# Kernel tuning notes

Hardware: AMD Instinct MI355X
Metric: run time of the kernel (lower is better)

The kernel has to match this reference:

```python
import jax, jax.numpy as jnp
import numpy as np

N_NODES = 100000
N_EDGES = 3200000
FEAT = 64  # pos(32) + vel(32)
OUT_DIM = 2


def setup_inputs() -> dict:
    key = jax.random.key(0)
    k1, k2, k3, k4, k5, k6, k7, k8 = jax.random.split(key, 8)
    pos = jax.random.normal(k1, (N_NODES, 32), dtype=jnp.float32)
    vel = jax.random.normal(k2, (N_NODES, 32), dtype=jnp.float32)
    edge_index = jax.random.randint(k3, (2, N_EDGES), 0, N_NODES, dtype=jnp.int64 if jax.config.jax_enable_x64 else jnp.int32)
    s = 1.0 / np.sqrt(FEAT)
    W_rel = jax.random.uniform(k4, (FEAT, FEAT), jnp.float32, -s, s)
    b_rel = jax.random.uniform(k5, (FEAT,), jnp.float32, -s, s)
    W_root = jax.random.uniform(k6, (FEAT, FEAT), jnp.float32, -s, s)
    W_pred = jax.random.uniform(k7, (FEAT, OUT_DIM), jnp.float32, -s, s)
    b_pred = jax.random.uniform(k8, (OUT_DIM,), jnp.float32, -s, s)
    return {"pos": pos, "vel": vel, "edge_index": edge_index,
            "W_rel": W_rel, "b_rel": b_rel, "W_root": W_root,
            "W_pred": W_pred, "b_pred": b_pred}


def reference(pos, vel, edge_index, W_rel, b_rel, W_root, W_pred, b_pred):
    # h = cat([pos, vel], -1)  -> [N, 64]
    h = jnp.concatenate([pos, vel], axis=-1)
    src, dst = edge_index[0], edge_index[1]
    # GraphConv (PyG, aggr='add'): out_i = lin_rel(sum_{j->i} h_j) + lin_root(h_i)
    msgs = h[src]  # [E, 64] irregular gather
    agg = jax.ops.segment_sum(msgs, dst, num_segments=N_NODES)  # [N, 64]
    conv_out = agg @ W_rel + b_rel + h @ W_root
    # lin_pred
    return conv_out @ W_pred + b_pred
```

## Files before the change

kernel.cpp:

```cpp
#include <hip/hip_runtime.h>

#define N_NODES 100000
#define N_EDGES 3200000
#define FEAT 64
#define OUT_DIM 2

#define SHIFT 8
#define S_NODES 256
#define K_BUCKETS 391
#define CAP 8704
#define NB 400
#define EPB (N_EDGES / NB)
#define BT 1024


__global__ __launch_bounds__(256) void node_kernel(const float* __restrict__ pos,
                                                   const float* __restrict__ vel,
                                                   const float* __restrict__ W_rel,
                                                   const float* __restrict__ b_rel,
                                                   const float* __restrict__ W_root,
                                                   const float* __restrict__ W_pred,
                                                   const float* __restrict__ b_pred,
                                                   float* __restrict__ y,
                                                   float* __restrict__ out,
                                                   int* __restrict__ gcount) {
    __shared__ float sM[258];
    int t = threadIdx.x;

    if (blockIdx.x == 0)
        for (int i = t; i < K_BUCKETS; i += 256) gcount[i] = 0;

    {
        const float* W = (t < 128) ? W_rel : W_root;
        int k = (t & 127) >> 1, o = t & 1;
        float acc = 0.f;
        #pragma unroll
        for (int f = 0; f < FEAT; ++f) acc += W[k * FEAT + f] * W_pred[f * OUT_DIM + o];
        sM[t] = acc;
        if (t < OUT_DIM) {
            float b = b_pred[t];
            #pragma unroll
            for (int f = 0; f < FEAT; ++f) b += b_rel[f] * W_pred[f * OUT_DIM + t];
            sM[256 + t] = b;
        }
    }
    __syncthreads();

    int n = blockIdx.x * 256 + t;
    if (n >= N_NODES) return;

    const float4* p4 = (const float4*)(pos + (size_t)n * 32);
    const float4* v4 = (const float4*)(vel + (size_t)n * 32);
    float h[FEAT];
    #pragma unroll
    for (int i = 0; i < 8; ++i) {
        float4 a = p4[i];
        h[i * 4 + 0] = a.x; h[i * 4 + 1] = a.y; h[i * 4 + 2] = a.z; h[i * 4 + 3] = a.w;
    }
    #pragma unroll
    for (int i = 0; i < 8; ++i) {
        float4 a = v4[i];
        h[32 + i * 4 + 0] = a.x; h[32 + i * 4 + 1] = a.y; h[32 + i * 4 + 2] = a.z; h[32 + i * 4 + 3] = a.w;
    }

    float rel0 = 0.f, rel1 = 0.f, ro0 = 0.f, ro1 = 0.f;
    #pragma unroll
    for (int k = 0; k < FEAT; ++k) {
        float hk = h[k];
        rel0 += hk * sM[2 * k + 0];
        rel1 += hk * sM[2 * k + 1];
        ro0  += hk * sM[128 + 2 * k + 0];
        ro1  += hk * sM[128 + 2 * k + 1];
    }
    ((float2*)y)[n]   = make_float2(rel0, rel1);
    ((float2*)out)[n] = make_float2(ro0 + sM[256], ro1 + sM[257]);
}

__global__ __launch_bounds__(BT) void binscatter_kernel(const int* __restrict__ edges,
                                                        int* __restrict__ gcount,
                                                        unsigned* __restrict__ scat) {
    __shared__ int hist[K_BUCKETS];
    __shared__ int cum[K_BUCKETS + 1];
    __shared__ int base[K_BUCKETS];
    __shared__ int pos[K_BUCKETS];
    __shared__ unsigned sortbuf[EPB];

    int t = threadIdx.x;
    for (int i = t; i < K_BUCKETS; i += BT) hist[i] = 0;
    __syncthreads();

    const int4* s4 = (const int4*)(edges) + blockIdx.x * (EPB / 4);
    const int4* d4 = (const int4*)(edges + N_EDGES) + blockIdx.x * (EPB / 4);
    int4 sreg[2], dreg[2];
    bool valid[2];
    #pragma unroll
    for (int r = 0; r < 2; ++r) {
        int i = t + r * BT;
        valid[r] = (i < EPB / 4);
        if (valid[r]) { sreg[r] = s4[i]; dreg[r] = d4[i]; }
    }

    #pragma unroll
    for (int r = 0; r < 2; ++r) {
        if (!valid[r]) continue;
        int4 d = dreg[r];
        atomicAdd(&hist[d.x >> SHIFT], 1);
        atomicAdd(&hist[d.y >> SHIFT], 1);
        atomicAdd(&hist[d.z >> SHIFT], 1);
        atomicAdd(&hist[d.w >> SHIFT], 1);
    }
    __syncthreads();

    for (int i = t; i < K_BUCKETS; i += BT) base[i] = atomicAdd(&gcount[i], hist[i]);
    if (t < 64) {
        int lo = t * 7;
        int vals[7];
        int lsum = 0;
        #pragma unroll
        for (int j = 0; j < 7; ++j) {
            int idx = lo + j;
            int v = (idx < K_BUCKETS) ? hist[idx] : 0;
            vals[j] = lsum;
            lsum += v;
        }
        int x = lsum;
        #pragma unroll
        for (int d = 1; d < 64; d <<= 1) {
            int up = __shfl_up(x, d);
            if (t >= d) x += up;
        }
        int excl = x - lsum;
        #pragma unroll
        for (int j = 0; j < 7; ++j) {
            int idx = lo + j;
            if (idx < K_BUCKETS) { cum[idx] = excl + vals[j]; pos[idx] = excl + vals[j]; }
        }
        if (t == 63) cum[K_BUCKETS] = excl + lsum;
    }
    __syncthreads();

    #pragma unroll
    for (int r = 0; r < 2; ++r) {
        if (!valid[r]) continue;
        int4 s = sreg[r];
        int4 d = dreg[r];
        int k, p;
        k = d.x >> SHIFT; p = atomicAdd(&pos[k], 1);
        sortbuf[p] = (unsigned)s.x | ((unsigned)(d.x & (S_NODES - 1)) << 17);
        k = d.y >> SHIFT; p = atomicAdd(&pos[k], 1);
        sortbuf[p] = (unsigned)s.y | ((unsigned)(d.y & (S_NODES - 1)) << 17);
        k = d.z >> SHIFT; p = atomicAdd(&pos[k], 1);
        sortbuf[p] = (unsigned)s.z | ((unsigned)(d.z & (S_NODES - 1)) << 17);
        k = d.w >> SHIFT; p = atomicAdd(&pos[k], 1);
        sortbuf[p] = (unsigned)s.w | ((unsigned)(d.w & (S_NODES - 1)) << 17);
    }
    __syncthreads();

    int wid = t >> 6, lane = t & 63;
    for (int k = wid; k < K_BUCKETS; k += BT / 64) {
        int s0 = cum[k], s1 = cum[k + 1], b = base[k];
        for (int j = s0 + lane; j < s1; j += 64) {
            int p = b + (j - s0);
            if (p < CAP) scat[(size_t)k * CAP + p] = sortbuf[j];
        }
    }
}

__global__ __launch_bounds__(BT) void accum_kernel(const unsigned* __restrict__ scat,
                                                   const int* __restrict__ gcount,
                                                   const float* __restrict__ y,
                                                   float* __restrict__ out) {
    __shared__ float acc[S_NODES * 2];
    int t = threadIdx.x;
    if (t < S_NODES * 2) acc[t] = 0.f;
    __syncthreads();

    int k = blockIdx.x;
    int c = gcount[k];
    if (c > CAP) c = CAP;
    const unsigned* sl = scat + (size_t)k * CAP;
    const float2* y2 = (const float2*)y;
    for (int i = t; i < c; i += BT) {
        unsigned p = sl[i];
        int src = p & 0x1FFFF;
        int dl = p >> 17;
        float2 v = y2[src];
        atomicAdd(&acc[dl], v.x);
        atomicAdd(&acc[S_NODES + dl], v.y);
    }
    __syncthreads();

    if (t < S_NODES) {
        int node = k * S_NODES + t;
        if (node < N_NODES) {
            float2* o2 = (float2*)out;
            float2 cv = o2[node];
            cv.x += acc[t];
            cv.y += acc[S_NODES + t];
            o2[node] = cv;
        }
    }
}

extern "C" void kernel_launch(void* const* d_in, const int* in_sizes, int n_in,
                              void* d_out, int out_size, void* d_ws, size_t ws_size,
                              hipStream_t stream) {
    const float* pos    = (const float*)d_in[0];
    const float* vel    = (const float*)d_in[1];
    const int*   edges  = (const int*)d_in[2];
    const float* W_rel  = (const float*)d_in[3];
    const float* b_rel  = (const float*)d_in[4];
    const float* W_root = (const float*)d_in[5];
    const float* W_pred = (const float*)d_in[6];
    const float* b_pred = (const float*)d_in[7];
    float* out = (float*)d_out;

    char* ws = (char*)d_ws;
    float*    y      = (float*)(ws + 2048);
    int*      gcount = (int*)(ws + 802048);
    unsigned* scat   = (unsigned*)(ws + 803712);

    int node_blocks = (N_NODES + 255) / 256;
    node_kernel<<<node_blocks, 256, 0, stream>>>(pos, vel, W_rel, b_rel, W_root,
                                                 W_pred, b_pred, y, out, gcount);

    binscatter_kernel<<<NB, BT, 0, stream>>>(edges, gcount, scat);

    accum_kernel<<<K_BUCKETS, BT, 0, stream>>>(scat, gcount, y, out);
}
```

Baseline: 165.5 us.

## Fuse node projection and edge binning into one launch; batch accum gathers

Merges the node projection kernel and the edge bucket-scatter kernel into a single launch. The first 98 blocks do the node work, the rest bin the edges, and shared memory is unioned between the two roles. Zeroing gcount moves to a memset. The accumulation kernel now loads packed edges as uint4 and issues all y gathers before the shared-memory atomics, which raises memory-level parallelism. The risks are an added memset launch, 1024-thread node blocks with fewer blocks in flight, and a fixed unroll of three uint4 loads per thread that relies on CAP fitting in 3*1024*4 entries.

```diff
diff --git a/kernel.cpp b/kernel.cpp
--- a/kernel.cpp
+++ b/kernel.cpp
@@ -12,85 +12,86 @@
 #define NB 400
 #define EPB (N_EDGES / NB)
 #define BT 1024
-
-
-__global__ __launch_bounds__(256) void node_kernel(const float* __restrict__ pos,
+#define NODE_BLOCKS 98
+
+
+__global__ __launch_bounds__(BT) void fused_kernel(const float* __restrict__ pos,
                                                    const float* __restrict__ vel,
                                                    const float* __restrict__ W_rel,
                                                    const float* __restrict__ b_rel,
                                                    const float* __restrict__ W_root,
                                                    const float* __restrict__ W_pred,
                                                    const float* __restrict__ b_pred,
+                                                   const int* __restrict__ edges,
+                                                   int* __restrict__ gcount,
+                                                   unsigned* __restrict__ scat,
                                                    float* __restrict__ y,
-                                                   float* __restrict__ out,
-                                                   int* __restrict__ gcount) {
-    __shared__ float sM[258];
+                                                   float* __restrict__ out) {
+    __shared__ union {
+        float sM[258];
+        struct {
+            int hist[K_BUCKETS];
+            int cum[K_BUCKETS + 1];
+            int base[K_BUCKETS];
+            int rpos[K_BUCKETS];
+            unsigned sortbuf[EPB];
+        } b;
+    } sm;
+
     int t = threadIdx.x;
 
-    if (blockIdx.x == 0)
-        for (int i = t; i < K_BUCKETS; i += 256) gcount[i] = 0;
-
-    {
-        const float* W = (t < 128) ? W_rel : W_root;
-        int k = (t & 127) >> 1, o = t & 1;
-        float acc = 0.f;
-        #pragma unroll
-        for (int f = 0; f < FEAT; ++f) acc += W[k * FEAT + f] * W_pred[f * OUT_DIM + o];
-        sM[t] = acc;
-        if (t < OUT_DIM) {
-            float b = b_pred[t];
+    if (blockIdx.x < NODE_BLOCKS) {
+        if (t < 256) {
+            const float* W = (t < 128) ? W_rel : W_root;
+            int k = (t & 127) >> 1, o = t & 1;
+            float acc = 0.f;
             #pragma unroll
-            for (int f = 0; f < FEAT; ++f) b += b_rel[f] * W_pred[f * OUT_DIM + t];
-            sM[256 + t] = b;
-        }
-    }
-    __syncthreads();
-
-    int n = blockIdx.x * 256 + t;
-    if (n >= N_NODES) return;
-
-    const float4* p4 = (const float4*)(pos + (size_t)n * 32);
-    const float4* v4 = (const float4*)(vel + (size_t)n * 32);
-    float h[FEAT];
-    #pragma unroll
-    for (int i = 0; i < 8; ++i) {
-        float4 a = p4[i];
-        h[i * 4 + 0] = a.x; h[i * 4 + 1] = a.y; h[i * 4 + 2] = a.z; h[i * 4 + 3] = a.w;
-    }
-    #pragma unroll
-    for (int i = 0; i < 8; ++i) {
-        float4 a = v4[i];
-        h[32 + i * 4 + 0] = a.x; h[32 + i * 4 + 1] = a.y; h[32 + i * 4 + 2] = a.z; h[32 + i * 4 + 3] = a.w;
-    }
-
-    float rel0 = 0.f, rel1 = 0.f, ro0 = 0.f, ro1 = 0.f;
-    #pragma unroll
-    for (int k = 0; k < FEAT; ++k) {
-        float hk = h[k];
-        rel0 += hk * sM[2 * k + 0];
-        rel1 += hk * sM[2 * k + 1];
-        ro0  += hk * sM[128 + 2 * k + 0];
-        ro1  += hk * sM[128 + 2 * k + 1];
-    }
-    ((float2*)y)[n]   = make_float2(rel0, rel1);
-    ((float2*)out)[n] = make_float2(ro0 + sM[256], ro1 + sM[257]);
-}
-
-__global__ __launch_bounds__(BT) void binscatter_kernel(const int* __restrict__ edges,
-                                                        int* __restrict__ gcount,
-                                                        unsigned* __restrict__ scat) {
-    __shared__ int hist[K_BUCKETS];
-    __shared__ int cum[K_BUCKETS + 1];
-    __shared__ int base[K_BUCKETS];
-    __shared__ int pos[K_BUCKETS];
-    __shared__ unsigned sortbuf[EPB];
-
-    int t = threadIdx.x;
-    for (int i = t; i < K_BUCKETS; i += BT) hist[i] = 0;
-    __syncthreads();
-
-    const int4* s4 = (const int4*)(edges) + blockIdx.x * (EPB / 4);
-    const int4* d4 = (const int4*)(edges + N_EDGES) + blockIdx.x * (EPB / 4);
+            for (int f = 0; f < FEAT; ++f) acc += W[k * FEAT + f] * W_pred[f * OUT_DIM + o];
+            sm.sM[t] = acc;
+            if (t < OUT_DIM) {
+                float b = b_pred[t];
+                #pragma unroll
+                for (int f = 0; f < FEAT; ++f) b += b_rel[f] * W_pred[f * OUT_DIM + t];
+                sm.sM[256 + t] = b;
+            }
+        }
+        __syncthreads();
+
+        int n = blockIdx.x * BT + t;
+        if (n >= N_NODES) return;
+
+        const float4* p4 = (const float4*)(pos + (size_t)n * 32);
+        const float4* v4 = (const float4*)(vel + (size_t)n * 32);
+        float rel0 = 0.f, rel1 = 0.f, ro0 = 0.f, ro1 = 0.f;
+        #pragma unroll
+        for (int i = 0; i < 8; ++i) {
+            float4 a = p4[i];
+            int k0 = i * 4;
+            rel0 += a.x * sm.sM[2*(k0+0)] + a.y * sm.sM[2*(k0+1)] + a.z * sm.sM[2*(k0+2)] + a.w * sm.sM[2*(k0+3)];
+            rel1 += a.x * sm.sM[2*(k0+0)+1] + a.y * sm.sM[2*(k0+1)+1] + a.z * sm.sM[2*(k0+2)+1] + a.w * sm.sM[2*(k0+3)+1];
+            ro0  += a.x * sm.sM[128+2*(k0+0)] + a.y * sm.sM[128+2*(k0+1)] + a.z * sm.sM[128+2*(k0+2)] + a.w * sm.sM[128+2*(k0+3)];
+            ro1  += a.x * sm.sM[128+2*(k0+0)+1] + a.y * sm.sM[128+2*(k0+1)+1] + a.z * sm.sM[128+2*(k0+2)+1] + a.w * sm.sM[128+2*(k0+3)+1];
+        }
+        #pragma unroll
+        for (int i = 0; i < 8; ++i) {
+            float4 a = v4[i];
+            int k0 = 32 + i * 4;
+            rel0 += a.x * sm.sM[2*(k0+0)] + a.y * sm.sM[2*(k0+1)] + a.z * sm.sM[2*(k0+2)] + a.w * sm.sM[2*(k0+3)];
+            rel1 += a.x * sm.sM[2*(k0+0)+1] + a.y * sm.sM[2*(k0+1)+1] + a.z * sm.sM[2*(k0+2)+1] + a.w * sm.sM[2*(k0+3)+1];
+            ro0  += a.x * sm.sM[128+2*(k0+0)] + a.y * sm.sM[128+2*(k0+1)] + a.z * sm.sM[128+2*(k0+2)] + a.w * sm.sM[128+2*(k0+3)];
+            ro1  += a.x * sm.sM[128+2*(k0+0)+1] + a.y * sm.sM[128+2*(k0+1)+1] + a.z * sm.sM[128+2*(k0+2)+1] + a.w * sm.sM[128+2*(k0+3)+1];
+        }
+        ((float2*)y)[n]   = make_float2(rel0, rel1);
+        ((float2*)out)[n] = make_float2(ro0 + sm.sM[256], ro1 + sm.sM[257]);
+        return;
+    }
+
+    int bb = blockIdx.x - NODE_BLOCKS;
+    for (int i = t; i < K_BUCKETS; i += BT) sm.b.hist[i] = 0;
+    __syncthreads();
+
+    const int4* s4 = (const int4*)(edges) + bb * (EPB / 4);
+    const int4* d4 = (const int4*)(edges + N_EDGES) + bb * (EPB / 4);
     int4 sreg[2], dreg[2];
     bool valid[2];
     #pragma unroll
@@ -104,14 +105,14 @@
     for (int r = 0; r < 2; ++r) {
         if (!valid[r]) continue;
         int4 d = dreg[r];
-        atomicAdd(&hist[d.x >> SHIFT], 1);
-        atomicAdd(&hist[d.y >> SHIFT], 1);
-        atomicAdd(&hist[d.z >> SHIFT], 1);
-        atomicAdd(&hist[d.w >> SHIFT], 1);
-    }
-    __syncthreads();
-
-    for (int i = t; i < K_BUCKETS; i += BT) base[i] = atomicAdd(&gcount[i], hist[i]);
+        atomicAdd(&sm.b.hist[d.x >> SHIFT], 1);
+        atomicAdd(&sm.b.hist[d.y >> SHIFT], 1);
+        atomicAdd(&sm.b.hist[d.z >> SHIFT], 1);
+        atomicAdd(&sm.b.hist[d.w >> SHIFT], 1);
+    }
+    __syncthreads();
+
+    for (int i = t; i < K_BUCKETS; i += BT) sm.b.base[i] = atomicAdd(&gcount[i], sm.b.hist[i]);
     if (t < 64) {
         int lo = t * 7;
         int vals[7];
@@ -119,7 +120,7 @@
         #pragma unroll
         for (int j = 0; j < 7; ++j) {
             int idx = lo + j;
-            int v = (idx < K_BUCKETS) ? hist[idx] : 0;
+            int v = (idx < K_BUCKETS) ? sm.b.hist[idx] : 0;
             vals[j] = lsum;
             lsum += v;
         }
@@ -133,9 +134,9 @@
         #pragma unroll
         for (int j = 0; j < 7; ++j) {
             int idx = lo + j;
-            if (idx < K_BUCKETS) { cum[idx] = excl + vals[j]; pos[idx] = excl + vals[j]; }
-        }
-        if (t == 63) cum[K_BUCKETS] = excl + lsum;
+            if (idx < K_BUCKETS) { sm.b.cum[idx] = excl + vals[j]; sm.b.rpos[idx] = excl + vals[j]; }
+        }
+        if (t == 63) sm.b.cum[K_BUCKETS] = excl + lsum;
     }
     __syncthreads();
 
@@ -145,23 +146,23 @@
         int4 s = sreg[r];
         int4 d = dreg[r];
         int k, p;
-        k = d.x >> SHIFT; p = atomicAdd(&pos[k], 1);
-        sortbuf[p] = (unsigned)s.x | ((unsigned)(d.x & (S_NODES - 1)) << 17);
-        k = d.y >> SHIFT; p = atomicAdd(&pos[k], 1);
-        sortbuf[p] = (unsigned)s.y | ((unsigned)(d.y & (S_NODES - 1)) << 17);
-        k = d.z >> SHIFT; p = atomicAdd(&pos[k], 1);
-        sortbuf[p] = (unsigned)s.z | ((unsigned)(d.z & (S_NODES - 1)) << 17);
-        k = d.w >> SHIFT; p = atomicAdd(&pos[k], 1);
-        sortbuf[p] = (unsigned)s.w | ((unsigned)(d.w & (S_NODES - 1)) << 17);
+        k = d.x >> SHIFT; p = atomicAdd(&sm.b.rpos[k], 1);
+        sm.b.sortbuf[p] = (unsigned)s.x | ((unsigned)(d.x & (S_NODES - 1)) << 17);
+        k = d.y >> SHIFT; p = atomicAdd(&sm.b.rpos[k], 1);
+        sm.b.sortbuf[p] = (unsigned)s.y | ((unsigned)(d.y & (S_NODES - 1)) << 17);
+        k = d.z >> SHIFT; p = atomicAdd(&sm.b.rpos[k], 1);
+        sm.b.sortbuf[p] = (unsigned)s.z | ((unsigned)(d.z & (S_NODES - 1)) << 17);
+        k = d.w >> SHIFT; p = atomicAdd(&sm.b.rpos[k], 1);
+        sm.b.sortbuf[p] = (unsigned)s.w | ((unsigned)(d.w & (S_NODES - 1)) << 17);
     }
     __syncthreads();
 
     int wid = t >> 6, lane = t & 63;
     for (int k = wid; k < K_BUCKETS; k += BT / 64) {
-        int s0 = cum[k], s1 = cum[k + 1], b = base[k];
+        int s0 = sm.b.cum[k], s1 = sm.b.cum[k + 1], b = sm.b.base[k];
         for (int j = s0 + lane; j < s1; j += 64) {
             int p = b + (j - s0);
-            if (p < CAP) scat[(size_t)k * CAP + p] = sortbuf[j];
+            if (p < CAP) scat[(size_t)k * CAP + p] = sm.b.sortbuf[j];
         }
     }
 }
@@ -170,23 +171,50 @@
                                                    const int* __restrict__ gcount,
                                                    const float* __restrict__ y,
                                                    float* __restrict__ out) {
-    __shared__ float acc[S_NODES * 2];
+    __shared__ float accx[S_NODES], accy[S_NODES];
     int t = threadIdx.x;
-    if (t < S_NODES * 2) acc[t] = 0.f;
+    if (t < S_NODES) { accx[t] = 0.f; accy[t] = 0.f; }
     __syncthreads();
 
     int k = blockIdx.x;
     int c = gcount[k];
     if (c > CAP) c = CAP;
-    const unsigned* sl = scat + (size_t)k * CAP;
+    const uint4* sl4 = (const uint4*)(scat + (size_t)k * CAP);
+    int nq = (c + 3) >> 2;
+
+    uint4 q0, q1, q2;
+    int i0 = t, i1 = t + BT, i2 = t + 2 * BT;
+    bool g0 = i0 < nq, g1 = i1 < nq, g2 = i2 < nq;
+    if (g0) q0 = sl4[i0];
+    if (g1) q1 = sl4[i1];
+    if (g2) q2 = sl4[i2];
+
     const float2* y2 = (const float2*)y;
-    for (int i = t; i < c; i += BT) {
-        unsigned p = sl[i];
-        int src = p & 0x1FFFF;
-        int dl = p >> 17;
-        float2 v = y2[src];
-        atomicAdd(&acc[dl], v.x);
-        atomicAdd(&acc[S_NODES + dl], v.y);
+    float2 v00, v01, v02, v03, v10, v11, v12, v13, v20, v21, v22, v23;
+    if (g0) { v00 = y2[q0.x & 0x1FFFF]; v01 = y2[q0.y & 0x1FFFF]; v02 = y2[q0.z & 0x1FFFF]; v03 = y2[q0.w & 0x1FFFF]; }
+    if (g1) { v10 = y2[q1.x & 0x1FFFF]; v11 = y2[q1.y & 0x1FFFF]; v12 = y2[q1.z & 0x1FFFF]; v13 = y2[q1.w & 0x1FFFF]; }
+    if (g2) { v20 = y2[q2.x & 0x1FFFF]; v21 = y2[q2.y & 0x1FFFF]; v22 = y2[q2.z & 0x1FFFF]; v23 = y2[q2.w & 0x1FFFF]; }
+
+    if (g0) {
+        int b = i0 << 2;
+        if (b + 0 < c) { atomicAdd(&accx[q0.x >> 17], v00.x); atomicAdd(&accy[q0.x >> 17], v00.y); }
+        if (b + 1 < c) { atomicAdd(&accx[q0.y >> 17], v01.x); atomicAdd(&accy[q0.y >> 17], v01.y); }
+        if (b + 2 < c) { atomicAdd(&accx[q0.z >> 17], v02.x); atomicAdd(&accy[q0.z >> 17], v02.y); }
+        if (b + 3 < c) { atomicAdd(&accx[q0.w >> 17], v03.x); atomicAdd(&accy[q0.w >> 17], v03.y); }
+    }
+    if (g1) {
+        int b = i1 << 2;
+        if (b + 0 < c) { atomicAdd(&accx[q1.x >> 17], v10.x); atomicAdd(&accy[q1.x >> 17], v10.y); }
+        if (b + 1 < c) { atomicAdd(&accx[q1.y >> 17], v11.x); atomicAdd(&accy[q1.y >> 17], v11.y); }
+        if (b + 2 < c) { atomicAdd(&accx[q1.z >> 17], v12.x); atomicAdd(&accy[q1.z >> 17], v12.y); }
+        if (b + 3 < c) { atomicAdd(&accx[q1.w >> 17], v13.x); atomicAdd(&accy[q1.w >> 17], v13.y); }
+    }
+    if (g2) {
+        int b = i2 << 2;
+        if (b + 0 < c) { atomicAdd(&accx[q2.x >> 17], v20.x); atomicAdd(&accy[q2.x >> 17], v20.y); }
+        if (b + 1 < c) { atomicAdd(&accx[q2.y >> 17], v21.x); atomicAdd(&accy[q2.y >> 17], v21.y); }
+        if (b + 2 < c) { atomicAdd(&accx[q2.z >> 17], v22.x); atomicAdd(&accy[q2.z >> 17], v22.y); }
+        if (b + 3 < c) { atomicAdd(&accx[q2.w >> 17], v23.x); atomicAdd(&accy[q2.w >> 17], v23.y); }
     }
     __syncthreads();
 
@@ -195,8 +223,8 @@
         if (node < N_NODES) {
             float2* o2 = (float2*)out;
             float2 cv = o2[node];
-            cv.x += acc[t];
-            cv.y += acc[S_NODES + t];
+            cv.x += accx[t];
+            cv.y += accy[t];
             o2[node] = cv;
         }
     }
@@ -220,11 +248,11 @@
     int*      gcount = (int*)(ws + 802048);
     unsigned* scat   = (unsigned*)(ws + 803712);
 
-    int node_blocks = (N_NODES + 255) / 256;
-    node_kernel<<<node_blocks, 256, 0, stream>>>(pos, vel, W_rel, b_rel, W_root,
-                                                 W_pred, b_pred, y, out, gcount);
-
-    binscatter_kernel<<<NB, BT, 0, stream>>>(edges, gcount, scat);
+    hipMemsetAsync(gcount, 0, K_BUCKETS * sizeof(int), stream);
+
+    fused_kernel<<<NODE_BLOCKS + NB, BT, 0, stream>>>(pos, vel, W_rel, b_rel, W_root,
+                                                      W_pred, b_pred, edges, gcount,
+                                                      scat, y, out);
 
     accum_kernel<<<K_BUCKETS, BT, 0, stream>>>(scat, gcount, y, out);
 }
```

Measured after the change: 168.1 us. No clear change (+1.6%).

## Fuse node, bin-scatter and accumulate stages into one cooperative kernel

Applied to the files above, without the earlier changes.

Merges the three launches into a single cooperative kernel of 256 blocks that separates the histogram, scatter and accumulate phases with grid-wide syncs. The bucketing changes to 256 buckets of 391 nodes each, so each block owns one bucket, keeps its root projection in registers, and writes the output once instead of doing a read-modify-write. The accumulate phase reads the scatter list with vectorized uint4 loads. It removes launch gaps and one pass over the output, but adds two grid barriers and a large shared-memory footprint per block, and keeps the three-kernel path as a fallback if the cooperative launch fails.

```diff
diff --git a/kernel.cpp b/kernel.cpp
--- a/kernel.cpp
+++ b/kernel.cpp
@@ -1,192 +1,362 @@
 #include <hip/hip_runtime.h>
+#include <hip/hip_cooperative_groups.h>
+
+namespace cg = cooperative_groups;
 
 #define N_NODES 100000
 #define N_EDGES 3200000
 #define FEAT 64
 #define OUT_DIM 2
 
-#define SHIFT 8
-#define S_NODES 256
-#define K_BUCKETS 391
-#define CAP 8704
-#define NB 400
-#define EPB (N_EDGES / NB)
+#define S_NODES 391
+#define K_BUCKETS 256
+#define CAP 13072
+#define GRID 256
 #define BT 1024
-
-
-__global__ __launch_bounds__(256) void node_kernel(const float* __restrict__ pos,
-                                                   const float* __restrict__ vel,
-                                                   const float* __restrict__ W_rel,
-                                                   const float* __restrict__ b_rel,
-                                                   const float* __restrict__ W_root,
-                                                   const float* __restrict__ W_pred,
-                                                   const float* __restrict__ b_pred,
-                                                   float* __restrict__ y,
-                                                   float* __restrict__ out,
-                                                   int* __restrict__ gcount) {
-    __shared__ float sM[258];
-    int t = threadIdx.x;
-
-    if (blockIdx.x == 0)
-        for (int i = t; i < K_BUCKETS; i += 256) gcount[i] = 0;
-
-    {
+#define EPB 12500
+#define NQ 3125
+#define V3LIM 53
+#define FB_NODE_BLOCKS 98
+
+
+__device__ __forceinline__ unsigned pack_edge(int s, int d) {
+    unsigned k = (unsigned)d / S_NODES;
+    unsigned dl = (unsigned)d - k * S_NODES;
+    return (unsigned)s | (dl << 17);
+}
+
+__device__ __forceinline__ void fold_weights(int t,
+        const float* __restrict__ W_rel, const float* __restrict__ b_rel,
+        const float* __restrict__ W_root, const float* __restrict__ W_pred,
+        const float* __restrict__ b_pred, float* sMl) {
+    if (t < 256) {
         const float* W = (t < 128) ? W_rel : W_root;
         int k = (t & 127) >> 1, o = t & 1;
         float acc = 0.f;
         #pragma unroll
         for (int f = 0; f < FEAT; ++f) acc += W[k * FEAT + f] * W_pred[f * OUT_DIM + o];
-        sM[t] = acc;
+        sMl[t] = acc;
         if (t < OUT_DIM) {
-            float b = b_pred[t];
+            float bb = b_pred[t];
             #pragma unroll
-            for (int f = 0; f < FEAT; ++f) b += b_rel[f] * W_pred[f * OUT_DIM + t];
-            sM[256 + t] = b;
-        }
-    }
-    __syncthreads();
-
-    int n = blockIdx.x * 256 + t;
-    if (n >= N_NODES) return;
-
+            for (int f = 0; f < FEAT; ++f) bb += b_rel[f] * W_pred[f * OUT_DIM + t];
+            sMl[256 + t] = bb;
+        }
+    }
+}
+
+__device__ __forceinline__ void node_dot(int n, const float* sMl,
+        const float* __restrict__ pos, const float* __restrict__ vel,
+        float* __restrict__ y, float* rx, float* ry) {
     const float4* p4 = (const float4*)(pos + (size_t)n * 32);
     const float4* v4 = (const float4*)(vel + (size_t)n * 32);
-    float h[FEAT];
+    float rel0 = 0.f, rel1 = 0.f, ro0 = 0.f, ro1 = 0.f;
     #pragma unroll
     for (int i = 0; i < 8; ++i) {
         float4 a = p4[i];
-        h[i * 4 + 0] = a.x; h[i * 4 + 1] = a.y; h[i * 4 + 2] = a.z; h[i * 4 + 3] = a.w;
+        int k0 = i * 4;
+        rel0 += a.x*sMl[2*k0]       + a.y*sMl[2*k0+2]     + a.z*sMl[2*k0+4]     + a.w*sMl[2*k0+6];
+        rel1 += a.x*sMl[2*k0+1]     + a.y*sMl[2*k0+3]     + a.z*sMl[2*k0+5]     + a.w*sMl[2*k0+7];
+        ro0  += a.x*sMl[128+2*k0]   + a.y*sMl[128+2*k0+2] + a.z*sMl[128+2*k0+4] + a.w*sMl[128+2*k0+6];
+        ro1  += a.x*sMl[128+2*k0+1] + a.y*sMl[128+2*k0+3] + a.z*sMl[128+2*k0+5] + a.w*sMl[128+2*k0+7];
     }
     #pragma unroll
     for (int i = 0; i < 8; ++i) {
         float4 a = v4[i];
-        h[32 + i * 4 + 0] = a.x; h[32 + i * 4 + 1] = a.y; h[32 + i * 4 + 2] = a.z; h[32 + i * 4 + 3] = a.w;
-    }
-
-    float rel0 = 0.f, rel1 = 0.f, ro0 = 0.f, ro1 = 0.f;
-    #pragma unroll
-    for (int k = 0; k < FEAT; ++k) {
-        float hk = h[k];
-        rel0 += hk * sM[2 * k + 0];
-        rel1 += hk * sM[2 * k + 1];
-        ro0  += hk * sM[128 + 2 * k + 0];
-        ro1  += hk * sM[128 + 2 * k + 1];
-    }
-    ((float2*)y)[n]   = make_float2(rel0, rel1);
-    ((float2*)out)[n] = make_float2(ro0 + sM[256], ro1 + sM[257]);
-}
-
-__global__ __launch_bounds__(BT) void binscatter_kernel(const int* __restrict__ edges,
-                                                        int* __restrict__ gcount,
-                                                        unsigned* __restrict__ scat) {
+        int k0 = 32 + i * 4;
+        rel0 += a.x*sMl[2*k0]       + a.y*sMl[2*k0+2]     + a.z*sMl[2*k0+4]     + a.w*sMl[2*k0+6];
+        rel1 += a.x*sMl[2*k0+1]     + a.y*sMl[2*k0+3]     + a.z*sMl[2*k0+5]     + a.w*sMl[2*k0+7];
+        ro0  += a.x*sMl[128+2*k0]   + a.y*sMl[128+2*k0+2] + a.z*sMl[128+2*k0+4] + a.w*sMl[128+2*k0+6];
+        ro1  += a.x*sMl[128+2*k0+1] + a.y*sMl[128+2*k0+3] + a.z*sMl[128+2*k0+5] + a.w*sMl[128+2*k0+7];
+    }
+    ((float2*)y)[n] = make_float2(rel0, rel1);
+    *rx = ro0 + sMl[256];
+    *ry = ro1 + sMl[257];
+}
+
+__global__ __launch_bounds__(BT, 4) void mega_kernel(
+        const float* __restrict__ pos, const float* __restrict__ vel,
+        const float* __restrict__ W_rel, const float* __restrict__ b_rel,
+        const float* __restrict__ W_root, const float* __restrict__ W_pred,
+        const float* __restrict__ b_pred, const int* __restrict__ edges,
+        int* __restrict__ gcount, unsigned* __restrict__ scat,
+        float* __restrict__ y, float* __restrict__ out) {
+    __shared__ float sMl[258];
     __shared__ int hist[K_BUCKETS];
     __shared__ int cum[K_BUCKETS + 1];
     __shared__ int base[K_BUCKETS];
-    __shared__ int pos[K_BUCKETS];
+    __shared__ int rpos[K_BUCKETS];
     __shared__ unsigned sortbuf[EPB];
-
-    int t = threadIdx.x;
+    __shared__ float accx[S_NODES], accy[S_NODES];
+
+    cg::grid_group grid = cg::this_grid();
+    const int t = threadIdx.x;
+    const int b = blockIdx.x;
+
     for (int i = t; i < K_BUCKETS; i += BT) hist[i] = 0;
-    __syncthreads();
-
-    const int4* s4 = (const int4*)(edges) + blockIdx.x * (EPB / 4);
-    const int4* d4 = (const int4*)(edges + N_EDGES) + blockIdx.x * (EPB / 4);
-    int4 sreg[2], dreg[2];
-    bool valid[2];
-    #pragma unroll
-    for (int r = 0; r < 2; ++r) {
-        int i = t + r * BT;
-        valid[r] = (i < EPB / 4);
-        if (valid[r]) { sreg[r] = s4[i]; dreg[r] = d4[i]; }
-    }
-
-    #pragma unroll
-    for (int r = 0; r < 2; ++r) {
-        if (!valid[r]) continue;
-        int4 d = dreg[r];
-        atomicAdd(&hist[d.x >> SHIFT], 1);
-        atomicAdd(&hist[d.y >> SHIFT], 1);
-        atomicAdd(&hist[d.z >> SHIFT], 1);
-        atomicAdd(&hist[d.w >> SHIFT], 1);
-    }
-    __syncthreads();
-
+
+    const int4* d4 = (const int4*)(edges + N_EDGES) + b * NQ;
+    int4 dreg0 = d4[t], dreg1 = d4[t + BT], dreg2 = d4[t + 2 * BT];
+    const bool v3 = t < V3LIM;
+    int4 dreg3;
+    if (v3) dreg3 = d4[t + 3 * BT];
+
+    if (b == 0)
+        for (int i = t; i < K_BUCKETS; i += BT) gcount[i] = 0;
+    __syncthreads();
+
+    atomicAdd(&hist[(unsigned)dreg0.x / S_NODES], 1);
+    atomicAdd(&hist[(unsigned)dreg0.y / S_NODES], 1);
+    atomicAdd(&hist[(unsigned)dreg0.z / S_NODES], 1);
+    atomicAdd(&hist[(unsigned)dreg0.w / S_NODES], 1);
+    atomicAdd(&hist[(unsigned)dreg1.x / S_NODES], 1);
+    atomicAdd(&hist[(unsigned)dreg1.y / S_NODES], 1);
+    atomicAdd(&hist[(unsigned)dreg1.z / S_NODES], 1);
+    atomicAdd(&hist[(unsigned)dreg1.w / S_NODES], 1);
+    atomicAdd(&hist[(unsigned)dreg2.x / S_NODES], 1);
+    atomicAdd(&hist[(unsigned)dreg2.y / S_NODES], 1);
+    atomicAdd(&hist[(unsigned)dreg2.z / S_NODES], 1);
+    atomicAdd(&hist[(unsigned)dreg2.w / S_NODES], 1);
+    if (v3) {
+        atomicAdd(&hist[(unsigned)dreg3.x / S_NODES], 1);
+        atomicAdd(&hist[(unsigned)dreg3.y / S_NODES], 1);
+        atomicAdd(&hist[(unsigned)dreg3.z / S_NODES], 1);
+        atomicAdd(&hist[(unsigned)dreg3.w / S_NODES], 1);
+    }
+
+    __threadfence();
+    grid.sync();
+    __threadfence();
+
+    fold_weights(t, W_rel, b_rel, W_root, W_pred, b_pred, sMl);
     for (int i = t; i < K_BUCKETS; i += BT) base[i] = atomicAdd(&gcount[i], hist[i]);
     if (t < 64) {
-        int lo = t * 7;
-        int vals[7];
-        int lsum = 0;
-        #pragma unroll
-        for (int j = 0; j < 7; ++j) {
-            int idx = lo + j;
-            int v = (idx < K_BUCKETS) ? hist[idx] : 0;
-            vals[j] = lsum;
-            lsum += v;
-        }
+        int lo = t * 4;
+        int vals[4]; int lsum = 0;
+        #pragma unroll
+        for (int j = 0; j < 4; ++j) { int v = hist[lo + j]; vals[j] = lsum; lsum += v; }
         int x = lsum;
         #pragma unroll
-        for (int d = 1; d < 64; d <<= 1) {
-            int up = __shfl_up(x, d);
-            if (t >= d) x += up;
-        }
+        for (int dd = 1; dd < 64; dd <<= 1) { int up = __shfl_up(x, dd); if (t >= dd) x += up; }
         int excl = x - lsum;
         #pragma unroll
-        for (int j = 0; j < 7; ++j) {
-            int idx = lo + j;
-            if (idx < K_BUCKETS) { cum[idx] = excl + vals[j]; pos[idx] = excl + vals[j]; }
-        }
+        for (int j = 0; j < 4; ++j) { cum[lo + j] = excl + vals[j]; rpos[lo + j] = excl + vals[j]; }
         if (t == 63) cum[K_BUCKETS] = excl + lsum;
     }
     __syncthreads();
 
+    float rootx = 0.f, rooty = 0.f;
+    const int n = b * S_NODES + t;
+    if (t < S_NODES && n < N_NODES)
+        node_dot(n, sMl, pos, vel, y, &rootx, &rooty);
+
+    const int4* s4 = (const int4*)(edges) + b * NQ;
+    int4 sreg0 = s4[t], sreg1 = s4[t + BT], sreg2 = s4[t + 2 * BT];
+    int4 sreg3;
+    if (v3) sreg3 = s4[t + 3 * BT];
+    {
+        int k, p;
+        k = (unsigned)dreg0.x / S_NODES; p = atomicAdd(&rpos[k], 1); sortbuf[p] = pack_edge(sreg0.x, dreg0.x);
+        k = (unsigned)dreg0.y / S_NODES; p = atomicAdd(&rpos[k], 1); sortbuf[p] = pack_edge(sreg0.y, dreg0.y);
+        k = (unsigned)dreg0.z / S_NODES; p = atomicAdd(&rpos[k], 1); sortbuf[p] = pack_edge(sreg0.z, dreg0.z);
+        k = (unsigned)dreg0.w / S_NODES; p = atomicAdd(&rpos[k], 1); sortbuf[p] = pack_edge(sreg0.w, dreg0.w);
+        k = (unsigned)dreg1.x / S_NODES; p = atomicAdd(&rpos[k], 1); sortbuf[p] = pack_edge(sreg1.x, dreg1.x);
+        k = (unsigned)dreg1.y / S_NODES; p = atomicAdd(&rpos[k], 1); sortbuf[p] = pack_edge(sreg1.y, dreg1.y);
+        k = (unsigned)dreg1.z / S_NODES; p = atomicAdd(&rpos[k], 1); sortbuf[p] = pack_edge(sreg1.z, dreg1.z);
+        k = (unsigned)dreg1.w / S_NODES; p = atomicAdd(&rpos[k], 1); sortbuf[p] = pack_edge(sreg1.w, dreg1.w);
+        k = (unsigned)dreg2.x / S_NODES; p = atomicAdd(&rpos[k], 1); sortbuf[p] = pack_edge(sreg2.x, dreg2.x);
+        k = (unsigned)dreg2.y / S_NODES; p = atomicAdd(&rpos[k], 1); sortbuf[p] = pack_edge(sreg2.y, dreg2.y);
+        k = (unsigned)dreg2.z / S_NODES; p = atomicAdd(&rpos[k], 1); sortbuf[p] = pack_edge(sreg2.z, dreg2.z);
+        k = (unsigned)dreg2.w / S_NODES; p = atomicAdd(&rpos[k], 1); sortbuf[p] = pack_edge(sreg2.w, dreg2.w);
+        if (v3) {
+            k = (unsigned)dreg3.x / S_NODES; p = atomicAdd(&rpos[k], 1); sortbuf[p] = pack_edge(sreg3.x, dreg3.x);
+            k = (unsigned)dreg3.y / S_NODES; p = atomicAdd(&rpos[k], 1); sortbuf[p] = pack_edge(sreg3.y, dreg3.y);
+            k = (unsigned)dreg3.z / S_NODES; p = atomicAdd(&rpos[k], 1); sortbuf[p] = pack_edge(sreg3.z, dreg3.z);
+            k = (unsigned)dreg3.w / S_NODES; p = atomicAdd(&rpos[k], 1); sortbuf[p] = pack_edge(sreg3.w, dreg3.w);
+        }
+    }
+    __syncthreads();
+
+    {
+        int wid = t >> 6, lane = t & 63;
+        for (int k = wid; k < K_BUCKETS; k += BT / 64) {
+            int s0 = cum[k], s1 = cum[k + 1], gb = base[k];
+            for (int j = s0 + lane; j < s1; j += 64) {
+                int p = gb + (j - s0);
+                if (p < CAP) scat[(size_t)k * CAP + p] = sortbuf[j];
+            }
+        }
+    }
+
+    __threadfence();
+    grid.sync();
+    __threadfence();
+
+    if (t < S_NODES) { accx[t] = 0.f; accy[t] = 0.f; }
+    __syncthreads();
+
+    int c = gcount[b];
+    if (c > CAP) c = CAP;
+    const int nq = (c + 3) >> 2;
+    const uint4* sl4 = (const uint4*)(scat + (size_t)b * CAP);
+    const float2* y2 = (const float2*)y;
     #pragma unroll
-    for (int r = 0; r < 2; ++r) {
-        if (!valid[r]) continue;
-        int4 s = sreg[r];
-        int4 d = dreg[r];
-        int k, p;
-        k = d.x >> SHIFT; p = atomicAdd(&pos[k], 1);
-        sortbuf[p] = (unsigned)s.x | ((unsigned)(d.x & (S_NODES - 1)) << 17);
-        k = d.y >> SHIFT; p = atomicAdd(&pos[k], 1);
-        sortbuf[p] = (unsigned)s.y | ((unsigned)(d.y & (S_NODES - 1)) << 17);
-        k = d.z >> SHIFT; p = atomicAdd(&pos[k], 1);
-        sortbuf[p] = (unsigned)s.z | ((unsigned)(d.z & (S_NODES - 1)) << 17);
-        k = d.w >> SHIFT; p = atomicAdd(&pos[k], 1);
-        sortbuf[p] = (unsigned)s.w | ((unsigned)(d.w & (S_NODES - 1)) << 17);
+    for (int r = 0; r < 4; ++r) {
+        int i = t + r * BT;
+        if (i < nq) {
+            uint4 q = sl4[i];
+            float2 w0 = y2[q.x & 0x1FFFF];
+            float2 w1 = y2[q.y & 0x1FFFF];
+            float2 w2 = y2[q.z & 0x1FFFF];
+            float2 w3 = y2[q.w & 0x1FFFF];
+            int e = i << 2;
+            if (e + 0 < c) { atomicAdd(&accx[q.x >> 17], w0.x); atomicAdd(&accy[q.x >> 17], w0.y); }
+            if (e + 1 < c) { atomicAdd(&accx[q.y >> 17], w1.x); atomicAdd(&accy[q.y >> 17], w1.y); }
+            if (e + 2 < c) { atomicAdd(&accx[q.z >> 17], w2.x); atomicAdd(&accy[q.z >> 17], w2.y); }
+            if (e + 3 < c) { atomicAdd(&accx[q.w >> 17], w3.x); atomicAdd(&accy[q.w >> 17], w3.y); }
+        }
+    }
+    __syncthreads();
+
+    if (t < S_NODES && n < N_NODES)
+        ((float2*)out)[n] = make_float2(rootx + accx[t], rooty + accy[t]);
+}
+
+__global__ __launch_bounds__(BT) void fb_node_kernel(
+        const float* __restrict__ pos, const float* __restrict__ vel,
+        const float* __restrict__ W_rel, const float* __restrict__ b_rel,
+        const float* __restrict__ W_root, const float* __restrict__ W_pred,
+        const float* __restrict__ b_pred, float* __restrict__ y,
+        float* __restrict__ out, int* __restrict__ gcount) {
+    __shared__ float sMl[258];
+    int t = threadIdx.x;
+    if (blockIdx.x == 0)
+        for (int i = t; i < K_BUCKETS; i += BT) gcount[i] = 0;
+    fold_weights(t, W_rel, b_rel, W_root, W_pred, b_pred, sMl);
+    __syncthreads();
+    int n = blockIdx.x * BT + t;
+    if (n < N_NODES) {
+        float rx, ry;
+        node_dot(n, sMl, pos, vel, y, &rx, &ry);
+        ((float2*)out)[n] = make_float2(rx, ry);
+    }
+}
+
+__global__ __launch_bounds__(BT) void fb_binscatter_kernel(
+        const int* __restrict__ edges, int* __restrict__ gcount,
+        unsigned* __restrict__ scat) {
+    __shared__ int hist[K_BUCKETS];
+    __shared__ int cum[K_BUCKETS + 1];
+    __shared__ int base[K_BUCKETS];
+    __shared__ int rpos[K_BUCKETS];
+    __shared__ unsigned sortbuf[EPB];
+    int t = threadIdx.x, b = blockIdx.x;
+    for (int i = t; i < K_BUCKETS; i += BT) hist[i] = 0;
+
+    const int4* s4 = (const int4*)(edges) + b * NQ;
+    const int4* d4 = (const int4*)(edges + N_EDGES) + b * NQ;
+    int4 dreg0 = d4[t], dreg1 = d4[t + BT], dreg2 = d4[t + 2 * BT];
+    int4 sreg0 = s4[t], sreg1 = s4[t + BT], sreg2 = s4[t + 2 * BT];
+    const bool v3 = t < V3LIM;
+    int4 dreg3, sreg3;
+    if (v3) { dreg3 = d4[t + 3 * BT]; sreg3 = s4[t + 3 * BT]; }
+    __syncthreads();
+
+    atomicAdd(&hist[(unsigned)dreg0.x / S_NODES], 1);
+    atomicAdd(&hist[(unsigned)dreg0.y / S_NODES], 1);
+    atomicAdd(&hist[(unsigned)dreg0.z / S_NODES], 1);
+    atomicAdd(&hist[(unsigned)dreg0.w / S_NODES], 1);
+    atomicAdd(&hist[(unsigned)dreg1.x / S_NODES], 1);
+    atomicAdd(&hist[(unsigned)dreg1.y / S_NODES], 1);
+    atomicAdd(&hist[(unsigned)dreg1.z / S_NODES], 1);
+    atomicAdd(&hist[(unsigned)dreg1.w / S_NODES], 1);
+    atomicAdd(&hist[(unsigned)dreg2.x / S_NODES], 1);
+    atomicAdd(&hist[(unsigned)dreg2.y / S_NODES], 1);
+    atomicAdd(&hist[(unsigned)dreg2.z / S_NODES], 1);
+    atomicAdd(&hist[(unsigned)dreg2.w / S_NODES], 1);
+    if (v3) {
+        atomicAdd(&hist[(unsigned)dreg3.x / S_NODES], 1);
+        atomicAdd(&hist[(unsigned)dreg3.y / S_NODES], 1);
+        atomicAdd(&hist[(unsigned)dreg3.z / S_NODES], 1);
+        atomicAdd(&hist[(unsigned)dreg3.w / S_NODES], 1);
+    }
+    __syncthreads();
+
+    for (int i = t; i < K_BUCKETS; i += BT) base[i] = atomicAdd(&gcount[i], hist[i]);
+    if (t < 64) {
+        int lo = t * 4;
+        int vals[4]; int lsum = 0;
+        #pragma unroll
+        for (int j = 0; j < 4; ++j) { int v = hist[lo + j]; vals[j] = lsum; lsum += v; }
+        int x = lsum;
+        #pragma unroll
+        for (int dd = 1; dd < 64; dd <<= 1) { int up = __shfl_up(x, dd); if (t >= dd) x += up; }
+        int excl = x - lsum;
+        #pragma unroll
+        for (int j = 0; j < 4; ++j) { cum[lo + j] = excl + vals[j]; rpos[lo + j] = excl + vals[j]; }
+        if (t == 63) cum[K_BUCKETS] = excl + lsum;
+    }
+    __syncthreads();
+
+    int k, p;
+    k = (unsigned)dreg0.x / S_NODES; p = atomicAdd(&rpos[k], 1); sortbuf[p] = pack_edge(sreg0.x, dreg0.x);
+    k = (unsigned)dreg0.y / S_NODES; p = atomicAdd(&rpos[k], 1); sortbuf[p] = pack_edge(sreg0.y, dreg0.y);
+    k = (unsigned)dreg0.z / S_NODES; p = atomicAdd(&rpos[k], 1); sortbuf[p] = pack_edge(sreg0.z, dreg0.z);
+    k = (unsigned)dreg0.w / S_NODES; p = atomicAdd(&rpos[k], 1); sortbuf[p] = pack_edge(sreg0.w, dreg0.w);
+    k = (unsigned)dreg1.x / S_NODES; p = atomicAdd(&rpos[k], 1); sortbuf[p] = pack_edge(sreg1.x, dreg1.x);
+    k = (unsigned)dreg1.y / S_NODES; p = atomicAdd(&rpos[k], 1); sortbuf[p] = pack_edge(sreg1.y, dreg1.y);
+    k = (unsigned)dreg1.z / S_NODES; p = atomicAdd(&rpos[k], 1); sortbuf[p] = pack_edge(sreg1.z, dreg1.z);
+    k = (unsigned)dreg1.w / S_NODES; p = atomicAdd(&rpos[k], 1); sortbuf[p] = pack_edge(sreg1.w, dreg1.w);
+    k = (unsigned)dreg2.x / S_NODES; p = atomicAdd(&rpos[k], 1); sortbuf[p] = pack_edge(sreg2.x, dreg2.x);
+    k = (unsigned)dreg2.y / S_NODES; p = atomicAdd(&rpos[k], 1); sortbuf[p] = pack_edge(sreg2.y, dreg2.y);
+    k = (unsigned)dreg2.z / S_NODES; p = atomicAdd(&rpos[k], 1); sortbuf[p] = pack_edge(sreg2.z, dreg2.z);
+    k = (unsigned)dreg2.w / S_NODES; p = atomicAdd(&rpos[k], 1); sortbuf[p] = pack_edge(sreg2.w, dreg2.w);
+    if (v3) {
+        k = (unsigned)dreg3.x / S_NODES; p = atomicAdd(&rpos[k], 1); sortbuf[p] = pack_edge(sreg3.x, dreg3.x);
+        k = (unsigned)dreg3.y / S_NODES; p = atomicAdd(&rpos[k], 1); sortbuf[p] = pack_edge(sreg3.y, dreg3.y);
+        k = (unsigned)dreg3.z / S_NODES; p = atomicAdd(&rpos[k], 1); sortbuf[p] = pack_edge(sreg3.z, dreg3.z);
+        k = (unsigned)dreg3.w / S_NODES; p = atomicAdd(&rpos[k], 1); sortbuf[p] = pack_edge(sreg3.w, dreg3.w);
     }
     __syncthreads();
 
     int wid = t >> 6, lane = t & 63;
-    for (int k = wid; k < K_BUCKETS; k += BT / 64) {
-        int s0 = cum[k], s1 = cum[k + 1], b = base[k];
+    for (int kk = wid; kk < K_BUCKETS; kk += BT / 64) {
+        int s0 = cum[kk], s1 = cum[kk + 1], gb = base[kk];
         for (int j = s0 + lane; j < s1; j += 64) {
-            int p = b + (j - s0);
-            if (p < CAP) scat[(size_t)k * CAP + p] = sortbuf[j];
-        }
-    }
-}
-
-__global__ __launch_bounds__(BT) void accum_kernel(const unsigned* __restrict__ scat,
-                                                   const int* __restrict__ gcount,
-                                                   const float* __restrict__ y,
-                                                   float* __restrict__ out) {
-    __shared__ float acc[S_NODES * 2];
-    int t = threadIdx.x;
-    if (t < S_NODES * 2) acc[t] = 0.f;
-    __syncthreads();
-
-    int k = blockIdx.x;
+            int pp = gb + (j - s0);
+            if (pp < CAP) scat[(size_t)kk * CAP + pp] = sortbuf[j];
+        }
+    }
+}
+
+__global__ __launch_bounds__(BT) void fb_accum_kernel(
+        const unsigned* __restrict__ scat, const int* __restrict__ gcount,
+        const float* __restrict__ y, float* __restrict__ out) {
+    __shared__ float accx[S_NODES], accy[S_NODES];
+    int t = threadIdx.x, k = blockIdx.x;
+    if (t < S_NODES) { accx[t] = 0.f; accy[t] = 0.f; }
+    __syncthreads();
+
     int c = gcount[k];
     if (c > CAP) c = CAP;
-    const unsigned* sl = scat + (size_t)k * CAP;
+    const int nq = (c + 3) >> 2;
+    const uint4* sl4 = (const uint4*)(scat + (size_t)k * CAP);
     const float2* y2 = (const float2*)y;
-    for (int i = t; i < c; i += BT) {
-        unsigned p = sl[i];
-        int src = p & 0x1FFFF;
-        int dl = p >> 17;
-        float2 v = y2[src];
-        atomicAdd(&acc[dl], v.x);
-        atomicAdd(&acc[S_NODES + dl], v.y);
+    #pragma unroll
+    for (int r = 0; r < 4; ++r) {
+        int i = t + r * BT;
+        if (i < nq) {
+            uint4 q = sl4[i];
+            float2 w0 = y2[q.x & 0x1FFFF];
+            float2 w1 = y2[q.y & 0x1FFFF];
+            float2 w2 = y2[q.z & 0x1FFFF];
+            float2 w3 = y2[q.w & 0x1FFFF];
+            int e = i << 2;
+            if (e + 0 < c) { atomicAdd(&accx[q.x >> 17], w0.x); atomicAdd(&accy[q.x >> 17], w0.y); }
+            if (e + 1 < c) { atomicAdd(&accx[q.y >> 17], w1.x); atomicAdd(&accy[q.y >> 17], w1.y); }
+            if (e + 2 < c) { atomicAdd(&accx[q.z >> 17], w2.x); atomicAdd(&accy[q.z >> 17], w2.y); }
+            if (e + 3 < c) { atomicAdd(&accx[q.w >> 17], w3.x); atomicAdd(&accy[q.w >> 17], w3.y); }
+        }
     }
     __syncthreads();
 
@@ -195,8 +365,8 @@
         if (node < N_NODES) {
             float2* o2 = (float2*)out;
             float2 cv = o2[node];
-            cv.x += acc[t];
-            cv.y += acc[S_NODES + t];
+            cv.x += accx[t];
+            cv.y += accy[t];
             o2[node] = cv;
         }
     }
@@ -218,13 +388,19 @@
     char* ws = (char*)d_ws;
     float*    y      = (float*)(ws + 2048);
     int*      gcount = (int*)(ws + 802048);
-    unsigned* scat   = (unsigned*)(ws + 803712);
-
-    int node_blocks = (N_NODES + 255) / 256;
-    node_kernel<<<node_blocks, 256, 0, stream>>>(pos, vel, W_rel, b_rel, W_root,
-                                                 W_pred, b_pred, y, out, gcount);
-
-    binscatter_kernel<<<NB, BT, 0, stream>>>(edges, gcount, scat);
-
-    accum_kernel<<<K_BUCKETS, BT, 0, stream>>>(scat, gcount, y, out);
-}
+    unsigned* scat   = (unsigned*)(ws + 804096);
+
+    void* args[12] = {(void*)&pos, (void*)&vel, (void*)&W_rel, (void*)&b_rel,
+                      (void*)&W_root, (void*)&W_pred, (void*)&b_pred, (void*)&edges,
+                      (void*)&gcount, (void*)&scat, (void*)&y, (void*)&out};
+
+    hipError_t err = hipLaunchCooperativeKernel((const void*)mega_kernel,
+                                                dim3(GRID), dim3(BT), args, 0, stream);
+    if (err != hipSuccess) {
+        fb_node_kernel<<<FB_NODE_BLOCKS, BT, 0, stream>>>(pos, vel, W_rel, b_rel,
+                                                          W_root, W_pred, b_pred,
+                                                          y, out, gcount);
+        fb_binscatter_kernel<<<K_BUCKETS, BT, 0, stream>>>(edges, gcount, scat);
+        fb_accum_kernel<<<K_BUCKETS, BT, 0, stream>>>(scat, gcount, y, out);
+    }
+}
```

Measured after the change: 483.4 us. +192.1%, slower.

## Gather projected values into bucket buffers as bf16 during binning

Applied to the files above, without the earlier changes.

The binning kernel now performs the y[src] gather itself when writing each edge to its bucket slot. It stores the two projected values packed as bf16 in one word, plus a separate byte array holding the local destination index. The accumulate kernel then streams contiguous vector loads with no random gather, at the cost of an extra byte buffer and reduced precision from bf16 rounding of messages. A fallback path keeps the old layout when the workspace is too small.

```diff
diff --git a/kernel.cpp b/kernel.cpp
--- a/kernel.cpp
+++ b/kernel.cpp
@@ -13,6 +13,7 @@
 #define EPB (N_EDGES / NB)
 #define BT 1024
 
+#define FAST_WS_NEEDED 17820032ull
 
 __global__ __launch_bounds__(256) void node_kernel(const float* __restrict__ pos,
                                                    const float* __restrict__ vel,
@@ -76,13 +77,16 @@
     ((float2*)out)[n] = make_float2(ro0 + sM[256], ro1 + sM[257]);
 }
 
+template <bool WITH_VAL>
 __global__ __launch_bounds__(BT) void binscatter_kernel(const int* __restrict__ edges,
                                                         int* __restrict__ gcount,
-                                                        unsigned* __restrict__ scat) {
+                                                        unsigned* __restrict__ scat,
+                                                        unsigned char* __restrict__ dlbuf,
+                                                        const float* __restrict__ y) {
     __shared__ int hist[K_BUCKETS];
     __shared__ int cum[K_BUCKETS + 1];
     __shared__ int base[K_BUCKETS];
-    __shared__ int pos[K_BUCKETS];
+    __shared__ int rpos[K_BUCKETS];
     __shared__ unsigned sortbuf[EPB];
 
     int t = threadIdx.x;
@@ -133,7 +137,7 @@
         #pragma unroll
         for (int j = 0; j < 7; ++j) {
             int idx = lo + j;
-            if (idx < K_BUCKETS) { cum[idx] = excl + vals[j]; pos[idx] = excl + vals[j]; }
+            if (idx < K_BUCKETS) { cum[idx] = excl + vals[j]; rpos[idx] = excl + vals[j]; }
         }
         if (t == 63) cum[K_BUCKETS] = excl + lsum;
     }
@@ -145,13 +149,13 @@
         int4 s = sreg[r];
         int4 d = dreg[r];
         int k, p;
-        k = d.x >> SHIFT; p = atomicAdd(&pos[k], 1);
+        k = d.x >> SHIFT; p = atomicAdd(&rpos[k], 1);
         sortbuf[p] = (unsigned)s.x | ((unsigned)(d.x & (S_NODES - 1)) << 17);
-        k = d.y >> SHIFT; p = atomicAdd(&pos[k], 1);
+        k = d.y >> SHIFT; p = atomicAdd(&rpos[k], 1);
         sortbuf[p] = (unsigned)s.y | ((unsigned)(d.y & (S_NODES - 1)) << 17);
-        k = d.z >> SHIFT; p = atomicAdd(&pos[k], 1);
+        k = d.z >> SHIFT; p = atomicAdd(&rpos[k], 1);
         sortbuf[p] = (unsigned)s.z | ((unsigned)(d.z & (S_NODES - 1)) << 17);
-        k = d.w >> SHIFT; p = atomicAdd(&pos[k], 1);
+        k = d.w >> SHIFT; p = atomicAdd(&rpos[k], 1);
         sortbuf[p] = (unsigned)s.w | ((unsigned)(d.w & (S_NODES - 1)) << 17);
     }
     __syncthreads();
@@ -161,32 +165,68 @@
         int s0 = cum[k], s1 = cum[k + 1], b = base[k];
         for (int j = s0 + lane; j < s1; j += 64) {
             int p = b + (j - s0);
-            if (p < CAP) scat[(size_t)k * CAP + p] = sortbuf[j];
-        }
-    }
-}
-
-__global__ __launch_bounds__(BT) void accum_kernel(const unsigned* __restrict__ scat,
-                                                   const int* __restrict__ gcount,
-                                                   const float* __restrict__ y,
-                                                   float* __restrict__ out) {
-    __shared__ float acc[S_NODES * 2];
-    int t = threadIdx.x;
-    if (t < S_NODES * 2) acc[t] = 0.f;
-    __syncthreads();
-
-    int k = blockIdx.x;
+            if (p < CAP) {
+                unsigned e = sortbuf[j];
+                if (WITH_VAL) {
+                    unsigned src = e & 0x1FFFF;
+                    unsigned long long uv = __builtin_nontemporal_load(
+                        (const unsigned long long*)y + src);
+                    unsigned bx = (unsigned)uv, by = (unsigned)(uv >> 32);
+                    bx += 0x7FFFu + ((bx >> 16) & 1u);
+                    by += 0x7FFFu + ((by >> 16) & 1u);
+                    scat[(size_t)k * CAP + p] = (bx >> 16) | (by & 0xFFFF0000u);
+                    dlbuf[(size_t)k * CAP + p] = (unsigned char)(e >> 17);
+                } else {
+                    scat[(size_t)k * CAP + p] = e;
+                }
+            }
+        }
+    }
+}
+
+__global__ __launch_bounds__(BT) void accum_fast_kernel(const unsigned* __restrict__ valbuf,
+                                                        const unsigned char* __restrict__ dlbuf,
+                                                        const int* __restrict__ gcount,
+                                                        float* __restrict__ out) {
+    __shared__ float accx[S_NODES], accy[S_NODES];
+    int t = threadIdx.x, k = blockIdx.x;
+    if (t < S_NODES) { accx[t] = 0.f; accy[t] = 0.f; }
+    __syncthreads();
+
     int c = gcount[k];
     if (c > CAP) c = CAP;
-    const unsigned* sl = scat + (size_t)k * CAP;
-    const float2* y2 = (const float2*)y;
-    for (int i = t; i < c; i += BT) {
-        unsigned p = sl[i];
-        int src = p & 0x1FFFF;
-        int dl = p >> 17;
-        float2 v = y2[src];
-        atomicAdd(&acc[dl], v.x);
-        atomicAdd(&acc[S_NODES + dl], v.y);
+    int nq = (c + 3) >> 2;
+    const uint4* v4 = (const uint4*)(valbuf + (size_t)k * CAP);
+    const unsigned* dl4 = (const unsigned*)(dlbuf + (size_t)k * CAP);
+
+    #pragma unroll
+    for (int r = 0; r < 3; ++r) {
+        int i = t + r * BT;
+        if (i < nq) {
+            uint4 q = v4[i];
+            unsigned dls = dl4[i];
+            int e = i << 2;
+            if (e + 0 < c) {
+                int dl = dls & 255;
+                atomicAdd(&accx[dl], __uint_as_float(q.x << 16));
+                atomicAdd(&accy[dl], __uint_as_float(q.x & 0xFFFF0000u));
+            }
+            if (e + 1 < c) {
+                int dl = (dls >> 8) & 255;
+                atomicAdd(&accx[dl], __uint_as_float(q.y << 16));
+                atomicAdd(&accy[dl], __uint_as_float(q.y & 0xFFFF0000u));
+            }
+            if (e + 2 < c) {
+                int dl = (dls >> 16) & 255;
+                atomicAdd(&accx[dl], __uint_as_float(q.z << 16));
+                atomicAdd(&accy[dl], __uint_as_float(q.z & 0xFFFF0000u));
+            }
+            if (e + 3 < c) {
+                int dl = (dls >> 24) & 255;
+                atomicAdd(&accx[dl], __uint_as_float(q.w << 16));
+                atomicAdd(&accy[dl], __uint_as_float(q.w & 0xFFFF0000u));
+            }
+        }
     }
     __syncthreads();
 
@@ -195,8 +235,43 @@
         if (node < N_NODES) {
             float2* o2 = (float2*)out;
             float2 cv = o2[node];
-            cv.x += acc[t];
-            cv.y += acc[S_NODES + t];
+            cv.x += accx[t];
+            cv.y += accy[t];
+            o2[node] = cv;
+        }
+    }
+}
+
+__global__ __launch_bounds__(BT) void accum_slow_kernel(const unsigned* __restrict__ scat,
+                                                        const int* __restrict__ gcount,
+                                                        const float* __restrict__ y,
+                                                        float* __restrict__ out) {
+    __shared__ float accx[S_NODES], accy[S_NODES];
+    int t = threadIdx.x, k = blockIdx.x;
+    if (t < S_NODES) { accx[t] = 0.f; accy[t] = 0.f; }
+    __syncthreads();
+
+    int c = gcount[k];
+    if (c > CAP) c = CAP;
+    const unsigned* sl = scat + (size_t)k * CAP;
+    for (int i = t; i < c; i += BT) {
+        unsigned p = sl[i];
+        int src = p & 0x1FFFF;
+        int dl = p >> 17;
+        unsigned long long uv = __builtin_nontemporal_load(
+            (const unsigned long long*)y + src);
+        atomicAdd(&accx[dl], __uint_as_float((unsigned)uv));
+        atomicAdd(&accy[dl], __uint_as_float((unsigned)(uv >> 32)));
+    }
+    __syncthreads();
+
+    if (t < S_NODES) {
+        int node = k * S_NODES + t;
+        if (node < N_NODES) {
+            float2* o2 = (float2*)out;
+            float2 cv = o2[node];
+            cv.x += accx[t];
+            cv.y += accy[t];
             o2[node] = cv;
         }
     }
@@ -216,15 +291,20 @@
     float* out = (float*)d_out;
 
     char* ws = (char*)d_ws;
-    float*    y      = (float*)(ws + 2048);
-    int*      gcount = (int*)(ws + 802048);
-    unsigned* scat   = (unsigned*)(ws + 803712);
+    float*         y      = (float*)(ws + 2048);
+    int*           gcount = (int*)(ws + 802048);
+    unsigned*      scat   = (unsigned*)(ws + 803712);
+    unsigned char* dlbuf  = (unsigned char*)(ws + 14416768);
 
     int node_blocks = (N_NODES + 255) / 256;
     node_kernel<<<node_blocks, 256, 0, stream>>>(pos, vel, W_rel, b_rel, W_root,
                                                  W_pred, b_pred, y, out, gcount);
 
-    binscatter_kernel<<<NB, BT, 0, stream>>>(edges, gcount, scat);
-
-    accum_kernel<<<K_BUCKETS, BT, 0, stream>>>(scat, gcount, y, out);
-}
+    if (ws_size >= FAST_WS_NEEDED) {
+        binscatter_kernel<true><<<NB, BT, 0, stream>>>(edges, gcount, scat, dlbuf, y);
+        accum_fast_kernel<<<K_BUCKETS, BT, 0, stream>>>(scat, dlbuf, gcount, out);
+    } else {
+        binscatter_kernel<false><<<NB, BT, 0, stream>>>(edges, gcount, scat, dlbuf, y);
+        accum_slow_kernel<<<K_BUCKETS, BT, 0, stream>>>(scat, gcount, y, out);
+    }
+}
```

New measurement: 219.2 us. 32.5% more time.
